# Optimization experiments

Hardware: AMD Instinct MI355X
Metric: run time of the kernel (lower is better)

Reference implementation:

```python
import jax, jax.numpy as jnp
import numpy as np

NUM_GRAPHS = 64
NEG_SLOPE_EDGE = 0.2   # GATLayer alpha
NEG_SLOPE_READ = 0.01  # torch default leaky_relu slope in ReadoutLayer


def leaky_relu(x, slope):
    return jnp.where(x >= 0, x, slope * x)


def segment_softmax(e, seg, n):
    # numerically stable softmax of edge logits grouped by destination node
    m = jax.ops.segment_max(e, seg, num_segments=n)
    m = jnp.where(jnp.isfinite(m), m, 0.0)  # guard nodes with no in-edges
    ex = jnp.exp(e - m[seg])
    s = jax.ops.segment_sum(ex, seg, num_segments=n)
    return ex / jnp.where(s > 0, s, 1.0)[seg]


def gat_layer(h, src, dst, e_feat, W, a):
    n = h.shape[0]
    out = W.shape[1]
    z = h @ W                                      # [N, out]
    a_src, a_dst, a_e = a[:out], a[out:2 * out], a[2 * out:]
    # concat([z_src, z_dst, e_feat]) @ a  ==  z_src@a_src + z_dst@a_dst + e@a_e
    logits = leaky_relu(z[src] @ a_src + z[dst] @ a_dst + e_feat @ a_e,
                        NEG_SLOPE_EDGE)            # [E]
    alpha = segment_softmax(logits, dst, n)        # [E]
    msg = alpha[:, None] * z[src]                  # [E, out]
    return jax.ops.segment_sum(msg, dst, num_segments=n)  # [N, out]


def readout(h, gid, w_att, b_att):
    # DGL mean_nodes(g, 'z', 'att'): multiply feat by weight, then mean per graph
    att = jnp.exp(leaky_relu(h @ w_att + b_att, NEG_SLOPE_READ))  # [N]
    num = jax.ops.segment_sum(att[:, None] * h, gid, num_segments=NUM_GRAPHS)
    cnt = jax.ops.segment_sum(jnp.ones_like(att), gid, num_segments=NUM_GRAPHS)
    return num / jnp.maximum(cnt, 1.0)[:, None]    # [G, hidden]


def setup_inputs() -> dict:
    key = jax.random.key(0)
    ks = jax.random.split(key, 16)
    N, E, F_IN, H, ED, C = 50000, 800000, 128, 128, 16, 10
    sc = lambda f: np.float32(1.0 / np.sqrt(f))
    return {
        "x": jax.random.normal(ks[0], (N, F_IN), jnp.float32),
        "e_feat": jax.random.normal(ks[1], (E, ED), jnp.float32),
        "src": jax.random.randint(ks[2], (E,), 0, N, dtype=jnp.int32),
        "dst": jax.random.randint(ks[3], (E,), 0, N, dtype=jnp.int32),
        "gid": jnp.sort(jax.random.randint(ks[4], (N,), 0, NUM_GRAPHS, dtype=jnp.int32)),
        "W1": jax.random.normal(ks[5], (F_IN, H), jnp.float32) * sc(F_IN),
        "a1": jax.random.normal(ks[6], (2 * H + ED,), jnp.float32) * sc(2 * H + ED),
        "W2": jax.random.normal(ks[7], (H, H), jnp.float32) * sc(H),
        "a2": jax.random.normal(ks[8], (2 * H + ED,), jnp.float32) * sc(2 * H + ED),
        "W3": jax.random.normal(ks[9], (H, H), jnp.float32) * sc(H),
        "a3": jax.random.normal(ks[10], (2 * H + ED,), jnp.float32) * sc(2 * H + ED),
        "w_att": jax.random.normal(ks[11], (H,), jnp.float32) * sc(H),
        "b_att": jnp.zeros((), jnp.float32),
        "W_cls": jax.random.normal(ks[12], (3 * H, C), jnp.float32) * sc(3 * H),
        "b_cls": jnp.zeros((C,), jnp.float32),
    }


def reference(x, e_feat, src, dst, gid, W1, a1, W2, a2, W3, a3,
              w_att, b_att, W_cls, b_cls):
    # dropout is identity at inference (training=False)
    h1 = jax.nn.relu(gat_layer(x, src, dst, e_feat, W1, a1))
    hg1 = readout(h1, gid, w_att, b_att)
    h2 = jax.nn.relu(gat_layer(h1, src, dst, e_feat, W2, a2))
    hg2 = readout(h2, gid, w_att, b_att)
    h3 = jax.nn.relu(gat_layer(h2, src, dst, e_feat, W3, a3))
    hg3 = readout(h3, gid, w_att, b_att)
    y = jnp.concatenate([hg1, hg2, hg3], axis=1) @ W_cls + b_cls  # [G, C]
    return jax.nn.log_softmax(y, axis=1)
```

## Files before the change

### kernel.cpp

```cpp
#include <hip/hip_runtime.h>
#include <math.h>

#define HD 128
#define ED 16
#define NG 64
#define NC 10
#define EPB_LOG 14
#define EPB (1<<EPB_LOG)

typedef short bf16x8 __attribute__((ext_vector_type(8)));
typedef float f32x4 __attribute__((ext_vector_type(4)));

__device__ __forceinline__ unsigned short f2b(float x){
  unsigned u = __float_as_uint(x);
  unsigned r = (u + 0x7fffu + ((u >> 16) & 1u)) >> 16;
  return (unsigned short)r;
}
__device__ __forceinline__ float blo(unsigned p){ return __uint_as_float(p << 16); }
__device__ __forceinline__ float bhi(unsigned p){ return __uint_as_float(p & 0xffff0000u); }
__device__ __forceinline__ float bperm_f(int idx, float v){
  return __int_as_float(__builtin_amdgcn_ds_bpermute(idx<<2, __float_as_int(v)));
}
__device__ __forceinline__ int bperm_i(int idx, int v){
  return __builtin_amdgcn_ds_bpermute(idx<<2, v);
}
__device__ __forceinline__ bf16x8 ld8f32_bf16(const float* p){
  float4 u0 = *(const float4*)p;
  float4 u1 = *(const float4*)(p+4);
  uint4 o;
  o.x = f2b(u0.x) | ((unsigned)f2b(u0.y)<<16);
  o.y = f2b(u0.z) | ((unsigned)f2b(u0.w)<<16);
  o.z = f2b(u1.x) | ((unsigned)f2b(u1.y)<<16);
  o.w = f2b(u1.z) | ((unsigned)f2b(u1.w)<<16);
  return __builtin_bit_cast(bf16x8, o);
}

__global__ __launch_bounds__(256) void k_hist(const int* __restrict__ dst,
                                              unsigned short* __restrict__ H16, int Nr2,
                                              int* __restrict__ rank, int E, int N){
  __shared__ unsigned hls[EPB/2];
  int kb = blockIdx.x;
  int e0 = kb << EPB_LOG;
  int e1 = e0 + EPB; if(e1 > E) e1 = E;
  int npass = (N + EPB - 1) >> EPB_LOG;
  for(int ps=0; ps<npass; ps++){
    int h0 = ps << EPB_LOG;
    for(int w=threadIdx.x; w<EPB/2; w+=256) hls[w] = 0u;
    __syncthreads();
    for(int e=e0+threadIdx.x; e<e1; e+=256){
      int d = dst[e];
      unsigned rel = (unsigned)(d - h0);
      if(rel < (unsigned)EPB){
        unsigned add = (rel & 1u) ? 0x10000u : 1u;
        unsigned old = atomicAdd(&hls[rel>>1], add);
        rank[e] = (int)((old >> ((rel & 1u)*16u)) & 0xffffu);
      }
    }
    __syncthreads();
    int nodes = N - h0; if(nodes > EPB) nodes = EPB;
    int words = (nodes + 1) >> 1;
    unsigned* Hg = (unsigned*)(H16 + (size_t)kb*Nr2 + h0);
    for(int w=threadIdx.x; w<words; w+=256) Hg[w] = hls[w];
    __syncthreads();
  }
}

__global__ __launch_bounds__(256) void k_pre(
    int NE4, int E,
    const int* __restrict__ src, const float* __restrict__ ef,
    const float* __restrict__ a1e, const float* __restrict__ a2e,
    const float* __restrict__ a3e, uint2* __restrict__ pay,
    const float* __restrict__ W1, const float* __restrict__ W2, const float* __restrict__ W3,
    unsigned short* __restrict__ Wb,
    const int* __restrict__ gid, float* __restrict__ cnt,
    float* __restrict__ hg,
    const unsigned short* __restrict__ H16, int Nr2, int NB,
    int* __restrict__ deg, int* __restrict__ bsum,
    int N){
  int b = blockIdx.x;
  if(b < NE4){
    int t = b*256 + threadIdx.x;
    int e = t >> 2;
    int sub = t & 3;
    if(e >= E) return;
    float4 f  = *(const float4*)&ef[(size_t)e*ED + sub*4];
    float4 A1 = *(const float4*)&a1e[sub*4];
    float4 A2 = *(const float4*)&a2e[sub*4];
    float4 A3 = *(const float4*)&a3e[sub*4];
    float q1 = fmaf(f.x,A1.x, fmaf(f.y,A1.y, fmaf(f.z,A1.z, f.w*A1.w)));
    float q2 = fmaf(f.x,A2.x, fmaf(f.y,A2.y, fmaf(f.z,A2.z, f.w*A2.w)));
    float q3 = fmaf(f.x,A3.x, fmaf(f.y,A3.y, fmaf(f.z,A3.z, f.w*A3.w)));
    q1 += __shfl_xor(q1,1); q1 += __shfl_xor(q1,2);
    q2 += __shfl_xor(q2,1); q2 += __shfl_xor(q2,2);
    q3 += __shfl_xor(q3,1); q3 += __shfl_xor(q3,2);
    if(sub == 0){
      uint2 A;
      A.x = (unsigned)f2b(q1) | ((unsigned)f2b(q2) << 16);
      A.y = (unsigned)src[e] | ((unsigned)f2b(q3) << 16);
      pay[e] = A;
    }
    return;
  }
  b -= NE4;
  if(b < 24){
    int idx = b*256 + threadIdx.x;
    if(idx >= 3*2048) return;
    int layer = idx >> 11;
    int r = idx & 2047;
    const float* W = (layer==0)?W1:((layer==1)?W2:W3);
    int lane = r & 63, tile = r >> 6;
    int kt = tile >> 3, nt = tile & 7;
    int qq = lane >> 4, cc = lane & 15;
    int kbase = kt*32 + qq*8;
    int col = nt*16 + cc;
    unsigned short tmp[8];
    #pragma unroll
    for(int j=0;j<8;j++) tmp[j] = f2b(W[(size_t)(kbase+j)*HD + col]);
    uint4 o;
    o.x = tmp[0]|((unsigned)tmp[1]<<16); o.y = tmp[2]|((unsigned)tmp[3]<<16);
    o.z = tmp[4]|((unsigned)tmp[5]<<16); o.w = tmp[6]|((unsigned)tmp[7]<<16);
    *(uint4*)&Wb[(size_t)idx*8] = o;
    return;
  }
  b -= 24;
  if(b == 0){
    int g = threadIdx.x;
    if(g >= NG) return;
    int lo=0, hi=N;
    while(lo<hi){ int mid=(lo+hi)>>1; if(gid[mid] < g) lo=mid+1; else hi=mid; }
    int start = lo; lo = start; hi = N;
    while(lo<hi){ int mid=(lo+hi)>>1; if(gid[mid] < g+1) lo=mid+1; else hi=mid; }
    cnt[g] = (float)(lo - start);
    return;
  }
  b -= 1;
  if(b < 24){
    int i = (b*256 + threadIdx.x)*4;
    if(i < 3*NG*HD) *(float4*)&hg[i] = (float4){0.f,0.f,0.f,0.f};
    return;
  }
  b -= 24;
  {
    __shared__ int rs[4];
    int i = b*256 + threadIdx.x;
    int s = 0;
    if(i < N){
      for(int k=0;k<NB;k++) s += (int)H16[(size_t)k*Nr2 + i];
      deg[i] = s;
    }
    #pragma unroll
    for(int o=32;o;o>>=1) s += __shfl_xor(s,o);
    if((threadIdx.x&63)==0) rs[threadIdx.x>>6] = s;
    __syncthreads();
    if(threadIdx.x==0) bsum[b] = rs[0]+rs[1]+rs[2]+rs[3];
  }
}

__global__ __launch_bounds__(256) void k_bprop2(const int* __restrict__ deg,
                                                const int* __restrict__ bsum,
                                                const unsigned short* __restrict__ H16, int Nr2,
                                                int* __restrict__ offs,
                                                int* __restrict__ offs2, int Nr,
                                                int N, int E, int NB){
  __shared__ int sh[256];
  __shared__ int sbase;
  int b = blockIdx.x, t = threadIdx.x;
  int s = 0;
  for(int j=t; j<b; j+=256) s += bsum[j];
  #pragma unroll
  for(int o=32;o;o>>=1) s += __shfl_xor(s,o);
  if(t < 4) sh[t] = 0;
  __syncthreads();
  if((t&63)==0) sh[t>>6] = s;
  __syncthreads();
  if(t==0) sbase = sh[0]+sh[1]+sh[2]+sh[3];
  __syncthreads();
  int i = b*256 + t;
  int v = (i<N) ? deg[i] : 0;
  sh[t] = v; __syncthreads();
  for(int o=1;o<256;o<<=1){ int u = (t>=o)?sh[t-o]:0; __syncthreads(); sh[t]+=u; __syncthreads(); }
  if(i<N){
    int base = sbase + sh[t] - v;
    offs[i] = base;
    int run = base;
    for(int k=0;k<NB;k++){
      offs2[(size_t)k*Nr + i] = run;
      run += (int)H16[(size_t)k*Nr2 + i];
    }
  }
  if(b==0 && t==0) offs[N] = E;
}


__device__ __forceinline__ void scatter_dev(int bidx,
                           const int* __restrict__ dst, const int* __restrict__ rank,
                           const uint2* __restrict__ pay,
                           const int* __restrict__ offs2, int Nr,
                           uint2* __restrict__ rec, int E){
  int e = bidx*256 + threadIdx.x;
  if(e >= E) return;
  int d = dst[e];
  int k = e >> EPB_LOG;
  int p = offs2[(size_t)k*Nr + d] + rank[e];
  rec[p] = pay[e];
}

__device__ __forceinline__ void gemm_dev(int bidx,
    const unsigned short* __restrict__ Ab,
    const float* __restrict__ Af,
    const unsigned short* __restrict__ Wb,
    unsigned short* __restrict__ Zb,
    const float* __restrict__ avec,
    float* __restrict__ ps, float* __restrict__ pd, int M)
{
  int tid = threadIdx.x;
  int w = tid >> 6, lane = tid & 63;
  int q = lane >> 4, c = lane & 15;
  int rowbase = bidx*128 + w*32;
  f32x4 acc[2][8];
  #pragma unroll
  for(int t=0;t<2;t++)
    #pragma unroll
    for(int n=0;n<8;n++) acc[t][n] = (f32x4){0.f,0.f,0.f,0.f};

  int r0 = rowbase + c;      if(r0 > M-1) r0 = M-1;
  int r1 = rowbase + 16 + c; if(r1 > M-1) r1 = M-1;
  #pragma unroll
  for(int kt=0; kt<4; kt++){
    int ko = kt*32 + q*8;
    bf16x8 a0, a1;
    if(Af){
      a0 = ld8f32_bf16(&Af[(size_t)r0*HD + ko]);
      a1 = ld8f32_bf16(&Af[(size_t)r1*HD + ko]);
    } else {
      a0 = __builtin_bit_cast(bf16x8, *(const uint4*)&Ab[(size_t)r0*HD + ko]);
      a1 = __builtin_bit_cast(bf16x8, *(const uint4*)&Ab[(size_t)r1*HD + ko]);
    }
    #pragma unroll
    for(int n=0;n<8;n++){
      bf16x8 b = __builtin_bit_cast(bf16x8, *(const uint4*)&Wb[(((size_t)(kt*8+n))*64 + lane)*8]);
      acc[0][n] = __builtin_amdgcn_mfma_f32_16x16x32_bf16(a0, b, acc[0][n], 0,0,0);
      acc[1][n] = __builtin_amdgcn_mfma_f32_16x16x32_bf16(a1, b, acc[1][n], 0,0,0);
    }
  }
  float asv[8], adv[8];
  #pragma unroll
  for(int n=0;n<8;n++){ asv[n] = avec[n*16+c]; adv[n] = avec[HD + n*16+c]; }
  #pragma unroll
  for(int t=0;t<2;t++){
    #pragma unroll
    for(int r=0;r<4;r++){
      int grow = rowbase + t*16 + 4*q + r;
      bool ok = grow < M;
      #pragma unroll
      for(int n=0;n<8;n++){
        if(ok) Zb[(size_t)grow*HD + n*16 + c] = f2b(acc[t][n][r]);
      }
      float pp = 0.f, dd = 0.f;
      #pragma unroll
      for(int n=0;n<8;n++){ pp = fmaf(acc[t][n][r], asv[n], pp); dd = fmaf(acc[t][n][r], adv[n], dd); }
      #pragma unroll
      for(int o=1;o<16;o<<=1){ pp += __shfl_xor(pp,o); dd += __shfl_xor(dd,o); }
      if(ok && c==0){ ps[grow] = pp; pd[grow] = dd; }
    }
  }
}

#define RCH 16
__device__ __forceinline__ void readout_dev(int rb,
                          const unsigned* __restrict__ hbu,
                          const float* __restrict__ att,
                          const int* __restrict__ gid,
                          float* __restrict__ hg, int N){
  int g = rb >> 2;
  int chunk = ((rb & 3) << 2) + (threadIdx.x >> 6);
  int t = threadIdx.x & 63;
  int lo=0, hi=N;
  while(lo<hi){ int mid=(lo+hi)>>1; if(gid[mid] < g) lo=mid+1; else hi=mid; }
  int start = lo; lo = start; hi = N;
  while(lo<hi){ int mid=(lo+hi)>>1; if(gid[mid] < g+1) lo=mid+1; else hi=mid; }
  int end = lo;
  int len = end - start;
  int c0 = start + (int)(((long long)len * chunk) / RCH);
  int c1 = start + (int)(((long long)len * (chunk+1)) / RCH);
  float acc0 = 0.f, acc1 = 0.f;
  for(int v=c0; v<c1; v++){
    unsigned P = hbu[(size_t)v*64 + t];
    float a = att[v];
    acc0 = fmaf(a, blo(P), acc0);
    acc1 = fmaf(a, bhi(P), acc1);
  }
  atomicAdd(&hg[g*HD + 2*t],     acc0);
  atomicAdd(&hg[g*HD + 2*t + 1], acc1);
}

__global__ __launch_bounds__(256) void k_sg1(
    const float* __restrict__ x, const unsigned short* __restrict__ Wb,
    unsigned short* __restrict__ Zb, const float* __restrict__ avec,
    float* __restrict__ ps, float* __restrict__ pd, int M, int GB,
    const int* __restrict__ dst, const int* __restrict__ rank,
    const uint2* __restrict__ pay,
    const int* __restrict__ offs2, int Nr, uint2* __restrict__ rec, int E){
  if(blockIdx.x < GB) gemm_dev(blockIdx.x, (const unsigned short*)0, x, Wb, Zb, avec, ps, pd, M);
  else scatter_dev(blockIdx.x - GB, dst, rank, pay, offs2, Nr, rec, E);
}

__global__ __launch_bounds__(256) void k_rg(
    const unsigned short* __restrict__ Ab, const unsigned short* __restrict__ Wb,
    unsigned short* __restrict__ Zb, const float* __restrict__ avec,
    float* __restrict__ ps, float* __restrict__ pd, int M, int GB,
    const unsigned* __restrict__ hbu, const float* __restrict__ att,
    const int* __restrict__ gid, float* __restrict__ hg, int N){
  if(blockIdx.x < GB) gemm_dev(blockIdx.x, Ab, (const float*)0, Wb, Zb, avec, ps, pd, M);
  else readout_dev(blockIdx.x - GB, hbu, att, gid, hg, N);
}

__global__ __launch_bounds__(256) void k_agg2(const uint4* __restrict__ zb4,
                                              const int* __restrict__ offs,
                                              const uint2* __restrict__ rec,
                                              const float* __restrict__ ps,
                                              const float* __restrict__ pd,
                                              int layer,
                                              unsigned* __restrict__ hbu,
                                              float* __restrict__ att,
                                              const float* __restrict__ watt,
                                              const float* __restrict__ batt, int N){
  int wid = blockIdx.x*4 + (threadIdx.x>>6);
  int lane = threadIdx.x & 63;
  if(wid >= N) return;
  int q = lane >> 4, c = lane & 15;
  int d0 = offs[wid], d1 = offs[wid+1];
  float pdv = pd[wid];
  float acc[8];
  #pragma unroll
  for(int i=0;i<8;i++) acc[i]=0.f;
  float ssum = 0.f;

  for(int t0=d0; t0<d1; t0+=64){
    int rem = d1 - t0; if(rem > 64) rem = 64;
    int j = t0 + lane;
    float w = 0.f; int u = 0;
    if(j < d1){
      uint2 R = rec[j];
      u = (int)(R.y & 0xffffu);
      unsigned qb = (layer==0) ? (R.x & 0xffffu) : (layer==1 ? (R.x >> 16) : (R.y >> 16));
      float ql = __uint_as_float(qb << 16);
      float l = ps[u] + pdv + ql;
      l = (l >= 0.f) ? l : 0.2f*l;
      w = __expf(l);
    }
    float ws = w;
    #pragma unroll
    for(int o=32;o;o>>=1) ws += __shfl_xor(ws,o);
    ssum += ws;
    for(int jb=0; jb<rem; jb+=16){
      float w0 = bperm_f(jb+q,    w);  int u0 = bperm_i(jb+q,    u);
      float w1 = bperm_f(jb+4+q,  w);  int u1 = bperm_i(jb+4+q,  u);
      float w2 = bperm_f(jb+8+q,  w);  int u2 = bperm_i(jb+8+q,  u);
      float w3 = bperm_f(jb+12+q, w);  int u3 = bperm_i(jb+12+q, u);
      uint4 P0 = zb4[(size_t)u0*16 + c];
      uint4 P1 = zb4[(size_t)u1*16 + c];
      uint4 P2 = zb4[(size_t)u2*16 + c];
      uint4 P3 = zb4[(size_t)u3*16 + c];
      acc[0] = fmaf(w0, blo(P0.x), acc[0]); acc[1] = fmaf(w0, bhi(P0.x), acc[1]);
      acc[2] = fmaf(w0, blo(P0.y), acc[2]); acc[3] = fmaf(w0, bhi(P0.y), acc[3]);
      acc[4] = fmaf(w0, blo(P0.z), acc[4]); acc[5] = fmaf(w0, bhi(P0.z), acc[5]);
      acc[6] = fmaf(w0, blo(P0.w), acc[6]); acc[7] = fmaf(w0, bhi(P0.w), acc[7]);
      acc[0] = fmaf(w1, blo(P1.x), acc[0]); acc[1] = fmaf(w1, bhi(P1.x), acc[1]);
      acc[2] = fmaf(w1, blo(P1.y), acc[2]); acc[3] = fmaf(w1, bhi(P1.y), acc[3]);
      acc[4] = fmaf(w1, blo(P1.z), acc[4]); acc[5] = fmaf(w1, bhi(P1.z), acc[5]);
      acc[6] = fmaf(w1, blo(P1.w), acc[6]); acc[7] = fmaf(w1, bhi(P1.w), acc[7]);
      acc[0] = fmaf(w2, blo(P2.x), acc[0]); acc[1] = fmaf(w2, bhi(P2.x), acc[1]);
      acc[2] = fmaf(w2, blo(P2.y), acc[2]); acc[3] = fmaf(w2, bhi(P2.y), acc[3]);
      acc[4] = fmaf(w2, blo(P2.z), acc[4]); acc[5] = fmaf(w2, bhi(P2.z), acc[5]);
      acc[6] = fmaf(w2, blo(P2.w), acc[6]); acc[7] = fmaf(w2, bhi(P2.w), acc[7]);
      acc[0] = fmaf(w3, blo(P3.x), acc[0]); acc[1] = fmaf(w3, bhi(P3.x), acc[1]);
      acc[2] = fmaf(w3, blo(P3.y), acc[2]); acc[3] = fmaf(w3, bhi(P3.y), acc[3]);
      acc[4] = fmaf(w3, blo(P3.z), acc[4]); acc[5] = fmaf(w3, bhi(P3.z), acc[5]);
      acc[6] = fmaf(w3, blo(P3.w), acc[6]); acc[7] = fmaf(w3, bhi(P3.w), acc[7]);
    }
  }
  #pragma unroll
  for(int i=0;i<8;i++){ acc[i] += __shfl_xor(acc[i],16); acc[i] += __shfl_xor(acc[i],32); }
  float inv = (d1 > d0) ? 1.0f/ssum : 0.0f;
  #pragma unroll
  for(int i=0;i<8;i++) acc[i] = fmaxf(acc[i]*inv, 0.f);
  hbu[(size_t)wid*64 + c*4 + q] = (unsigned)f2b(acc[2*q]) | ((unsigned)f2b(acc[2*q+1])<<16);
  float4 w0v = *(const float4*)&watt[c*8];
  float4 w1v = *(const float4*)&watt[c*8+4];
  float t = acc[0]*w0v.x + acc[1]*w0v.y + acc[2]*w0v.z + acc[3]*w0v.w
          + acc[4]*w1v.x + acc[5]*w1v.y + acc[6]*w1v.z + acc[7]*w1v.w;
  #pragma unroll
  for(int o=1;o<16;o<<=1) t += __shfl_xor(t,o);
  t += batt[0];
  float lr = (t >= 0.f) ? t : 0.01f*t;
  if(lane==0) att[wid] = __expf(lr);
}

__global__ __launch_bounds__(64) void k_readout(const unsigned* __restrict__ hbu,
                                                const float* __restrict__ att,
                                                const int* __restrict__ gid,
                                                float* __restrict__ hg, int N){
  int g = blockIdx.x / RCH;
  int chunk = blockIdx.x % RCH;
  int t = threadIdx.x;
  int lo=0, hi=N;
  while(lo<hi){ int mid=(lo+hi)>>1; if(gid[mid] < g) lo=mid+1; else hi=mid; }
  int start = lo; lo = start; hi = N;
  while(lo<hi){ int mid=(lo+hi)>>1; if(gid[mid] < g+1) lo=mid+1; else hi=mid; }
  int end = lo;
  int len = end - start;
  int c0 = start + (int)(((long long)len * chunk) / RCH);
  int c1 = start + (int)(((long long)len * (chunk+1)) / RCH);
  float acc0 = 0.f, acc1 = 0.f;
  for(int v=c0; v<c1; v++){
    unsigned P = hbu[(size_t)v*64 + t];
    float a = att[v];
    acc0 = fmaf(a, blo(P), acc0);
    acc1 = fmaf(a, bhi(P), acc1);
  }
  atomicAdd(&hg[g*HD + 2*t],     acc0);
  atomicAdd(&hg[g*HD + 2*t + 1], acc1);
}

__global__ __launch_bounds__(384) void k_final(const float* __restrict__ hg,
                                               const float* __restrict__ cnt,
                                               const float* __restrict__ Wc,
                                               const float* __restrict__ bc,
                                               float* __restrict__ out){
  int g = blockIdx.x;
  int t = threadIdx.x;
  __shared__ float red[6];
  __shared__ float yv[NC];
  float invc = 1.f / fmaxf(cnt[g], 1.f);
  int part = t >> 7;
  int f = t & 127;
  float v = hg[(size_t)part*NG*HD + g*HD + f] * invc;
  for(int c=0; c<NC; c++){
    float p = v * Wc[(size_t)t*NC + c];
    #pragma unroll
    for(int o=32;o;o>>=1) p += __shfl_xor(p,o);
    if((t&63)==0) red[t>>6] = p;
    __syncthreads();
    if(t==0) yv[c] = bc[c] + red[0]+red[1]+red[2]+red[3]+red[4]+red[5];
    __syncthreads();
  }
  if(t==0){
    float mx = -INFINITY;
    #pragma unroll
    for(int c=0;c<NC;c++) mx = fmaxf(mx, yv[c]);
    float s = 0.f;
    #pragma unroll
    for(int c=0;c<NC;c++) s += __expf(yv[c] - mx);
    float ls = logf(s);
    #pragma unroll
    for(int c=0;c<NC;c++) out[g*NC + c] = yv[c] - mx - ls;
  }
}

extern "C" void kernel_launch(void* const* d_in, const int* in_sizes, int n_in,
                              void* d_out, int out_size, void* d_ws, size_t ws_size,
                              hipStream_t stream) {
  const float* x     = (const float*)d_in[0];
  const float* efeat = (const float*)d_in[1];
  const int*   src   = (const int*)d_in[2];
  const int*   dst   = (const int*)d_in[3];
  const int*   gid   = (const int*)d_in[4];
  const float* W1    = (const float*)d_in[5];
  const float* a1    = (const float*)d_in[6];
  const float* W2    = (const float*)d_in[7];
  const float* a2    = (const float*)d_in[8];
  const float* W3    = (const float*)d_in[9];
  const float* a3    = (const float*)d_in[10];
  const float* watt  = (const float*)d_in[11];
  const float* batt  = (const float*)d_in[12];
  const float* Wc    = (const float*)d_in[13];
  const float* bc    = (const float*)d_in[14];
  float* out = (float*)d_out;

  int N = in_sizes[4];
  int E = in_sizes[2];
  int Nr = (N + 63) & ~63;
  int NB = (E + EPB - 1) >> EPB_LOG;
  int NP = (N + EPB - 1) >> EPB_LOG;
  int Nr2 = NP << EPB_LOG;

  char* p = (char*)d_ws;
  auto alloc = [&](size_t bytes)->void*{
    void* r = (void*)p;
    p += (bytes + 255) & ~(size_t)255;
    return r;
  };
  unsigned short* Hb = (unsigned short*)alloc((size_t)N*HD*2);
  unsigned short* Zb = (unsigned short*)alloc((size_t)N*HD*2);
  unsigned short* Wball = (unsigned short*)alloc((size_t)3*2048*8*2);
  float* ps      = (float*)alloc((size_t)N*4);
  float* pd      = (float*)alloc((size_t)N*4);
  float* att     = (float*)alloc((size_t)N*4);
  int*   deg     = (int*)  alloc((size_t)N*4);
  int*   offs    = (int*)  alloc((size_t)(N+1)*4);
  int*   offs2   = (int*)  alloc((size_t)NB*Nr*4);
  unsigned short* H16 = (unsigned short*)alloc((size_t)NB*Nr2*2);
  int*   rank    = (int*)  alloc((size_t)E*4);
  uint2* pay     = (uint2*)alloc((size_t)E*8);
  uint2* rec     = (uint2*)alloc((size_t)E*8);
  int*   bsum    = (int*)  alloc((size_t)1024*4);
  float* hg      = (float*)alloc((size_t)3*NG*HD*4);
  float* cnt     = (float*)alloc((size_t)NG*4);
  (void)ws_size; (void)n_in; (void)out_size;

  int nwblocks = (N + 3) / 4;
  int nb = (N + 255) / 256;
  int NE4 = (E*4 + 255) / 256;
  int GB = (N + 127) / 128;
  int SB = (E + 255) / 256;

  k_hist<<<NB, 256, 0, stream>>>(dst, H16, Nr2, rank, E, N);
  k_pre<<<NE4 + 24 + 1 + 24 + nb, 256, 0, stream>>>(NE4, E,
                                                    src, efeat, a1+2*HD, a2+2*HD, a3+2*HD, pay,
                                                    W1, W2, W3, Wball,
                                                    gid, cnt, hg,
                                                    H16, Nr2, NB, deg, bsum, N);
  k_bprop2<<<nb, 256, 0, stream>>>(deg, bsum, H16, Nr2, offs, offs2, Nr, N, E, NB);
  k_sg1<<<GB + SB, 256, 0, stream>>>(x, Wball, Zb, a1, ps, pd, N, GB,
                                     dst, rank, pay, offs2, Nr, rec, E);
  k_agg2<<<nwblocks, 256, 0, stream>>>((const uint4*)Zb, offs, rec, ps, pd, 0,
                                       (unsigned*)Hb, att, watt, batt, N);
  k_rg<<<GB + NG*4, 256, 0, stream>>>(Hb, Wball + (size_t)1*2048*8, Zb, a2, ps, pd, N, GB,
                                      (const unsigned*)Hb, att, gid, hg + 0*NG*HD, N);
  k_agg2<<<nwblocks, 256, 0, stream>>>((const uint4*)Zb, offs, rec, ps, pd, 1,
                                       (unsigned*)Hb, att, watt, batt, N);
  k_rg<<<GB + NG*4, 256, 0, stream>>>(Hb, Wball + (size_t)2*2048*8, Zb, a3, ps, pd, N, GB,
                                      (const unsigned*)Hb, att, gid, hg + 1*NG*HD, N);
  k_agg2<<<nwblocks, 256, 0, stream>>>((const uint4*)Zb, offs, rec, ps, pd, 2,
                                       (unsigned*)Hb, att, watt, batt, N);
  k_readout<<<NG*RCH, 64, 0, stream>>>((const unsigned*)Hb, att, gid,
                                       hg + 2*NG*HD, N);
  k_final<<<NG, 384, 0, stream>>>(hg, cnt, Wc, bc, out);
}
```

Baseline: 448.6 us.

## Split histogram passes across blocks and fuse into pre kernel

The per-edge-chunk histogram kernel is folded into k_pre, and its sequential loop over node ranges becomes one block per (edge chunk, node range) pair. This gives the histogram more parallelism and lets it run alongside the edge-payload, weight-conversion and zeroing work, which do not depend on it. The degree-sum part, which does depend on the histogram, moves into a new k_degsum kernel. Each histogram block now rereads its edge chunk's dst values once, and the launch count stays the same.

```diff
diff --git a/kernel.cpp b/kernel.cpp
--- a/kernel.cpp
+++ b/kernel.cpp
@@ -35,15 +35,24 @@
   return __builtin_bit_cast(bf16x8, o);
 }
 
-__global__ __launch_bounds__(256) void k_hist(const int* __restrict__ dst,
-                                              unsigned short* __restrict__ H16, int Nr2,
-                                              int* __restrict__ rank, int E, int N){
+__global__ __launch_bounds__(256) void k_pre(
+    const int* __restrict__ dst, unsigned short* __restrict__ H16, int Nr2,
+    int* __restrict__ rank, int NBH, int NP,
+    int NE4, int E,
+    const int* __restrict__ src, const float* __restrict__ ef,
+    const float* __restrict__ a1e, const float* __restrict__ a2e,
+    const float* __restrict__ a3e, uint2* __restrict__ pay,
+    const float* __restrict__ W1, const float* __restrict__ W2, const float* __restrict__ W3,
+    unsigned short* __restrict__ Wb,
+    const int* __restrict__ gid, float* __restrict__ cnt,
+    float* __restrict__ hg,
+    int N){
   __shared__ unsigned hls[EPB/2];
-  int kb = blockIdx.x;
-  int e0 = kb << EPB_LOG;
-  int e1 = e0 + EPB; if(e1 > E) e1 = E;
-  int npass = (N + EPB - 1) >> EPB_LOG;
-  for(int ps=0; ps<npass; ps++){
+  int b = blockIdx.x;
+  if(b < NBH){
+    int kb = b / NP, ps = b - kb*NP;
+    int e0 = kb << EPB_LOG;
+    int e1 = e0 + EPB; if(e1 > E) e1 = E;
     int h0 = ps << EPB_LOG;
     for(int w=threadIdx.x; w<EPB/2; w+=256) hls[w] = 0u;
     __syncthreads();
@@ -58,26 +67,14 @@
     }
     __syncthreads();
     int nodes = N - h0; if(nodes > EPB) nodes = EPB;
-    int words = (nodes + 1) >> 1;
-    unsigned* Hg = (unsigned*)(H16 + (size_t)kb*Nr2 + h0);
-    for(int w=threadIdx.x; w<words; w+=256) Hg[w] = hls[w];
-    __syncthreads();
-  }
-}
-
-__global__ __launch_bounds__(256) void k_pre(
-    int NE4, int E,
-    const int* __restrict__ src, const float* __restrict__ ef,
-    const float* __restrict__ a1e, const float* __restrict__ a2e,
-    const float* __restrict__ a3e, uint2* __restrict__ pay,
-    const float* __restrict__ W1, const float* __restrict__ W2, const float* __restrict__ W3,
-    unsigned short* __restrict__ Wb,
-    const int* __restrict__ gid, float* __restrict__ cnt,
-    float* __restrict__ hg,
-    const unsigned short* __restrict__ H16, int Nr2, int NB,
-    int* __restrict__ deg, int* __restrict__ bsum,
-    int N){
-  int b = blockIdx.x;
+    if(nodes > 0){
+      int words = (nodes + 1) >> 1;
+      unsigned* Hg = (unsigned*)(H16 + (size_t)kb*Nr2 + h0);
+      for(int w=threadIdx.x; w<words; w+=256) Hg[w] = hls[w];
+    }
+    return;
+  }
+  b -= NBH;
   if(b < NE4){
     int t = b*256 + threadIdx.x;
     int e = t >> 2;
@@ -134,26 +131,27 @@
     return;
   }
   b -= 1;
-  if(b < 24){
-    int i = (b*256 + threadIdx.x)*4;
-    if(i < 3*NG*HD) *(float4*)&hg[i] = (float4){0.f,0.f,0.f,0.f};
-    return;
-  }
-  b -= 24;
-  {
-    __shared__ int rs[4];
-    int i = b*256 + threadIdx.x;
-    int s = 0;
-    if(i < N){
-      for(int k=0;k<NB;k++) s += (int)H16[(size_t)k*Nr2 + i];
-      deg[i] = s;
-    }
-    #pragma unroll
-    for(int o=32;o;o>>=1) s += __shfl_xor(s,o);
-    if((threadIdx.x&63)==0) rs[threadIdx.x>>6] = s;
-    __syncthreads();
-    if(threadIdx.x==0) bsum[b] = rs[0]+rs[1]+rs[2]+rs[3];
-  }
+  int i = (b*256 + threadIdx.x)*4;
+  if(i < 3*NG*HD) *(float4*)&hg[i] = (float4){0.f,0.f,0.f,0.f};
+}
+
+__global__ __launch_bounds__(256) void k_degsum(const unsigned short* __restrict__ H16,
+                                                int Nr2, int NB,
+                                                int* __restrict__ deg,
+                                                int* __restrict__ bsum, int N){
+  __shared__ int rs[4];
+  int b = blockIdx.x;
+  int i = b*256 + threadIdx.x;
+  int s = 0;
+  if(i < N){
+    for(int k=0;k<NB;k++) s += (int)H16[(size_t)k*Nr2 + i];
+    deg[i] = s;
+  }
+  #pragma unroll
+  for(int o=32;o;o>>=1) s += __shfl_xor(s,o);
+  if((threadIdx.x&63)==0) rs[threadIdx.x>>6] = s;
+  __syncthreads();
+  if(threadIdx.x==0) bsum[b] = rs[0]+rs[1]+rs[2]+rs[3];
 }
 
 __global__ __launch_bounds__(256) void k_bprop2(const int* __restrict__ deg,
@@ -483,6 +481,7 @@
   int Nr = (N + 63) & ~63;
   int NB = (E + EPB - 1) >> EPB_LOG;
   int NP = (N + EPB - 1) >> EPB_LOG;
+  int NBH = NB * NP;
   int Nr2 = NP << EPB_LOG;
 
   char* p = (char*)d_ws;
@@ -515,12 +514,12 @@
   int GB = (N + 127) / 128;
   int SB = (E + 255) / 256;
 
-  k_hist<<<NB, 256, 0, stream>>>(dst, H16, Nr2, rank, E, N);
-  k_pre<<<NE4 + 24 + 1 + 24 + nb, 256, 0, stream>>>(NE4, E,
-                                                    src, efeat, a1+2*HD, a2+2*HD, a3+2*HD, pay,
-                                                    W1, W2, W3, Wball,
-                                                    gid, cnt, hg,
-                                                    H16, Nr2, NB, deg, bsum, N);
+  k_pre<<<NBH + NE4 + 24 + 1 + 24, 256, 0, stream>>>(dst, H16, Nr2, rank, NBH, NP,
+                                                     NE4, E,
+                                                     src, efeat, a1+2*HD, a2+2*HD, a3+2*HD, pay,
+                                                     W1, W2, W3, Wball,
+                                                     gid, cnt, hg, N);
+  k_degsum<<<nb, 256, 0, stream>>>(H16, Nr2, NB, deg, bsum, N);
   k_bprop2<<<nb, 256, 0, stream>>>(deg, bsum, H16, Nr2, offs, offs2, Nr, N, E, NB);
   k_sg1<<<GB + SB, 256, 0, stream>>>(x, Wball, Zb, a1, ps, pd, N, GB,
                                      dst, rank, pay, offs2, Nr, rec, E);
```

Measured after the change: 397.8 us. -11.3%, faster.
